# Kernel optimization log

Measured on AMD Instinct MI355X. Metric: run time of the kernel, lower is better.

The kernel has to match this reference:

```python
import jax, jax.numpy as jnp
import numpy as np

N = 20000      # num nodes
E = 320000     # num edges (avg degree 16)
F_IN = 518     # object_feature_dim
D = 128        # node_embedding_dim (= GAT out_channels)
ED = 32        # edge_embedding_dim
R = 26         # num_relations
H = 4          # GAT heads (concat=False -> mean over heads)
HID = 256      # node_encoder hidden


def _gat_layer(x, src, dst, ea, lin, lin_e, att_s, att_d, att_e, bias):
    """PyG GATConv: add_self_loops=True (fill_value='mean'), concat=False, negative_slope=0.2."""
    n = x.shape[0]
    ones = jnp.ones((src.shape[0],), x.dtype)
    cnt = jax.ops.segment_sum(ones, dst, num_segments=n)                    # [N]
    loop_ea = jax.ops.segment_sum(ea, dst, num_segments=n) / jnp.maximum(cnt, 1.0)[:, None]
    idx = jnp.arange(n)
    s = jnp.concatenate([src, idx])
    d = jnp.concatenate([dst, idx])
    ea2 = jnp.concatenate([ea, loop_ea], axis=0)                            # [E+N, ED]
    h = (x @ lin).reshape(n, H, D)                                          # [N,H,D]
    a_s = jnp.einsum('nhd,hd->nh', h, att_s)                                # [N,H]
    a_d = jnp.einsum('nhd,hd->nh', h, att_d)
    e = (ea2 @ lin_e).reshape(-1, H, D)                                     # [E+N,H,D]
    a_e = jnp.einsum('ehd,hd->eh', e, att_e)
    alpha = jax.nn.leaky_relu(a_s[s] + a_d[d] + a_e, 0.2)                   # [E+N,H]
    amax = jax.ops.segment_max(alpha, d, num_segments=n)
    alpha = jnp.exp(alpha - amax[d])
    denom = jax.ops.segment_sum(alpha, d, num_segments=n)
    alpha = alpha / (denom[d] + 1e-16)                                      # segment softmax
    msg = h[s] * alpha[:, :, None]                                          # [E+N,H,D]
    out = jax.ops.segment_sum(msg, d, num_segments=n)                       # [N,H,D]
    return out.mean(axis=1) + bias                                          # concat=False


def setup_inputs() -> dict:
    key = jax.random.key(0)
    ks = jax.random.split(key, 18)
    g = lambda k, shp, s=0.05: jax.random.normal(k, shp, jnp.float32) * s
    return {
        'x': g(ks[0], (N, F_IN), 1.0),
        'edge_index': jax.random.randint(ks[1], (2, E), 0, N),
        'edge_type': jax.random.randint(ks[2], (E,), 0, R),
        'w1': g(ks[3], (F_IN, HID)), 'b1': jnp.zeros((HID,), jnp.float32),
        'w2': g(ks[4], (HID, D)),    'b2': jnp.zeros((D,), jnp.float32),
        'rel_emb': g(ks[5], (R, ED), 1.0),
        'lin1': g(ks[6], (D, H * D)), 'line1': g(ks[7], (ED, H * D)),
        'atts1': g(ks[8], (H, D)), 'attd1': g(ks[9], (H, D)), 'atte1': g(ks[10], (H, D)),
        'bias1': jnp.zeros((D,), jnp.float32),
        'lin2': g(ks[11], (D, H * D)), 'line2': g(ks[12], (ED, H * D)),
        'atts2': g(ks[13], (H, D)), 'attd2': g(ks[14], (H, D)), 'atte2': g(ks[15], (H, D)),
        'bias2': jnp.zeros((D,), jnp.float32),
    }


def reference(x, edge_index, edge_type, w1, b1, w2, b2, rel_emb,
              lin1, line1, atts1, attd1, atte1, bias1,
              lin2, line2, atts2, attd2, atte2, bias2):
    src, dst = edge_index[0], edge_index[1]
    # node encoder (dropout inactive in eval)
    h = jax.nn.relu(x @ w1 + b1) @ w2 + b2                                  # [N,D]
    ea = rel_emb[edge_type]                                                 # [E,ED]
    h = jax.nn.relu(_gat_layer(h, src, dst, ea, lin1, line1, atts1, attd1, atte1, bias1))
    h = jax.nn.relu(_gat_layer(h, src, dst, ea, lin2, line2, atts2, attd2, atte2, bias2))
    return h
```

## Files before the change

kernel.cpp:

```cpp
#include <hip/hip_runtime.h>
#include <math.h>

#define N_NODES 20000
#define MP      20032
#define N_EDGES 320000
#define F_IN    518
#define HIDDEN  256
#define DIM     128
#define NH      4

typedef __attribute__((ext_vector_type(8))) short bf16x8;
typedef __attribute__((ext_vector_type(4))) float f32x4;
typedef unsigned short ushort_t;

__device__ __forceinline__ float lrelu02(float x) { return x > 0.f ? x : 0.2f * x; }

__device__ __forceinline__ void gl_lds16(const void* g, void* l) {
    __builtin_amdgcn_global_load_lds(
        (const __attribute__((address_space(1))) unsigned int*)g,
        (__attribute__((address_space(3))) unsigned int*)l, 16, 0, 0);
}

__device__ __forceinline__ unsigned int hi16(float v) { return __float_as_uint(v) >> 16; }
__device__ __forceinline__ unsigned int lo16(float v) {
    unsigned int h = __float_as_uint(v) & 0xFFFF0000u;
    return __float_as_uint(v - __uint_as_float(h)) >> 16;
}
__device__ __forceinline__ unsigned int rnd16(float v) {
    unsigned int u = __float_as_uint(v);
    return (u + 0x7FFFu + ((u >> 16) & 1u)) >> 16;
}
__device__ __forceinline__ float bfl(unsigned int u) { return __uint_as_float(u << 16); }
__device__ __forceinline__ float bfh(unsigned int u) { return __uint_as_float(u & 0xFFFF0000u); }

__global__ __launch_bounds__(256, 4) void gemm_mfma_v2(
    const ushort_t* __restrict__ Ah, const ushort_t* __restrict__ Al,
    const ushort_t* __restrict__ Bh, const ushort_t* __restrict__ Bl,
    const float* __restrict__ bias,
    int M, int K8, int N, int act,
    float* __restrict__ Cf,
    ushort_t* __restrict__ Ch, ushort_t* __restrict__ Cl,
    ushort_t* __restrict__ Cb,
    ushort_t* __restrict__ Ca)
{
    __shared__ __align__(16) ushort_t lds[12288];
    const int tid = threadIdx.x;
    const int w = tid >> 6, lane = tid & 63;
    const int row0 = blockIdx.y * 64, col0 = blockIdx.x * 128;
    const int nkb = K8 >> 2;
    const int m16 = lane & 15, q = lane >> 4;
    const bool use_al = (Al != nullptr);

    f32x4 acc[4][2] = {};

    for (int kb = 0; kb < nkb; ++kb) {
        const size_t kc = (size_t)(kb * 4 + w);
        const size_t aoff = (kc * MP + row0) * 8 + lane * 8;
        const size_t boff = (kc * N + col0) * 8 + lane * 8;
        gl_lds16(Ah + aoff, &lds[w * 512]);
        if (use_al) gl_lds16(Al + aoff, &lds[2048 + w * 512]);
        gl_lds16(Bh + boff,       &lds[4096 + w * 1024]);
        gl_lds16(Bh + boff + 512, &lds[4096 + w * 1024 + 512]);
        gl_lds16(Bl + boff,       &lds[8192 + w * 1024]);
        gl_lds16(Bl + boff + 512, &lds[8192 + w * 1024 + 512]);
        __syncthreads();

        bf16x8 fah[4], fal[4], fbh[2], fbl[2];
        const int fa = q * 512 + m16 * 8;
        #pragma unroll
        for (int mi = 0; mi < 4; ++mi) {
            fah[mi] = *(const bf16x8*)&lds[fa + mi * 128];
            if (use_al) fal[mi] = *(const bf16x8*)&lds[2048 + fa + mi * 128];
        }
        const int fb = q * 1024 + (w * 32 + m16) * 8;
        #pragma unroll
        for (int ni = 0; ni < 2; ++ni) {
            fbh[ni] = *(const bf16x8*)&lds[4096 + fb + ni * 128];
            fbl[ni] = *(const bf16x8*)&lds[8192 + fb + ni * 128];
        }
        #pragma unroll
        for (int mi = 0; mi < 4; ++mi)
            #pragma unroll
            for (int ni = 0; ni < 2; ++ni) {
                acc[mi][ni] = __builtin_amdgcn_mfma_f32_16x16x32_bf16(fah[mi], fbh[ni], acc[mi][ni], 0, 0, 0);
                acc[mi][ni] = __builtin_amdgcn_mfma_f32_16x16x32_bf16(fah[mi], fbl[ni], acc[mi][ni], 0, 0, 0);
            }
        if (use_al) {
            #pragma unroll
            for (int mi = 0; mi < 4; ++mi)
                #pragma unroll
                for (int ni = 0; ni < 2; ++ni)
                    acc[mi][ni] = __builtin_amdgcn_mfma_f32_16x16x32_bf16(fal[mi], fbh[ni], acc[mi][ni], 0, 0, 0);
        }
        __syncthreads();
    }

    #pragma unroll
    for (int ni = 0; ni < 2; ++ni) {
        const int col = col0 + w * 32 + ni * 16 + m16;
        const float bb = bias ? bias[col] : 0.f;
        #pragma unroll
        for (int mi = 0; mi < 4; ++mi) {
            #pragma unroll
            for (int r = 0; r < 4; ++r) {
                const int row = row0 + mi * 16 + q * 4 + r;
                if (row < M) {
                    float v = acc[mi][ni][r] + bb;
                    if (act) v = fmaxf(v, 0.f);
                    if (Cf) Cf[(size_t)row * N + col] = v;
                    if (Cb) Cb[(size_t)row * N + col] = (ushort_t)rnd16(v);
                    const size_t p = (((size_t)(col >> 3)) * MP + row) * 8 + (col & 7);
                    if (Ch) { Ch[p] = (ushort_t)hi16(v); Cl[p] = (ushort_t)lo16(v); }
                    if (Ca) Ca[p] = (ushort_t)rnd16(v);
                }
            }
        }
    }
}

__global__ __launch_bounds__(256, 3) void enc_fused_kernel(
    const ushort_t* __restrict__ Ah, const ushort_t* __restrict__ Al,
    const ushort_t* __restrict__ B1h, const ushort_t* __restrict__ B1l,
    const ushort_t* __restrict__ B2h, const ushort_t* __restrict__ B2l,
    const float* __restrict__ b1, const float* __restrict__ b2,
    float* __restrict__ Cf, ushort_t* __restrict__ Ca)
{
    __shared__ __align__(16) ushort_t lds[24576];
    const int tid = threadIdx.x;
    const int w = tid >> 6, lane = tid & 63;
    const int row0 = blockIdx.x * 64;
    const int m16 = lane & 15, q = lane >> 4;

    f32x4 acc1[4][4] = {};
    for (int kb = 0; kb < 17; ++kb) {
        const size_t kc = (size_t)(kb * 4 + w);
        const size_t aoff = (kc * MP + row0) * 8 + lane * 8;
        const size_t boff = kc * 2048 + lane * 8;
        gl_lds16(Ah + aoff, &lds[w * 512]);
        gl_lds16(Al + aoff, &lds[2048 + w * 512]);
        #pragma unroll
        for (int u = 0; u < 4; ++u) {
            gl_lds16(B1h + boff + u * 512, &lds[4096 + w * 2048 + u * 512]);
            gl_lds16(B1l + boff + u * 512, &lds[12288 + w * 2048 + u * 512]);
        }
        __syncthreads();

        bf16x8 fah[4], fal[4], fbh[4], fbl[4];
        const int fa = q * 512 + m16 * 8;
        #pragma unroll
        for (int mi = 0; mi < 4; ++mi) {
            fah[mi] = *(const bf16x8*)&lds[fa + mi * 128];
            fal[mi] = *(const bf16x8*)&lds[2048 + fa + mi * 128];
        }
        #pragma unroll
        for (int ni = 0; ni < 4; ++ni) {
            const int fb = q * 2048 + (ni * 64 + w * 16 + m16) * 8;
            fbh[ni] = *(const bf16x8*)&lds[4096 + fb];
            fbl[ni] = *(const bf16x8*)&lds[12288 + fb];
        }
        #pragma unroll
        for (int mi = 0; mi < 4; ++mi)
            #pragma unroll
            for (int ni = 0; ni < 4; ++ni) {
                acc1[mi][ni] = __builtin_amdgcn_mfma_f32_16x16x32_bf16(fah[mi], fbh[ni], acc1[mi][ni], 0, 0, 0);
                acc1[mi][ni] = __builtin_amdgcn_mfma_f32_16x16x32_bf16(fah[mi], fbl[ni], acc1[mi][ni], 0, 0, 0);
                acc1[mi][ni] = __builtin_amdgcn_mfma_f32_16x16x32_bf16(fal[mi], fbh[ni], acc1[mi][ni], 0, 0, 0);
            }
        __syncthreads();
    }

    float b1c[4];
    #pragma unroll
    for (int ni = 0; ni < 4; ++ni) b1c[ni] = b1[ni * 64 + w * 16 + m16];

    f32x4 acc2[4][2] = {};
    const int kc2l = w * 2 + (m16 >> 3);
    const int k7 = m16 & 7;
    for (int st = 0; st < 4; ++st) {
        #pragma unroll
        for (int mi = 0; mi < 4; ++mi)
            #pragma unroll
            for (int r = 0; r < 4; ++r) {
                const float v = fmaxf(acc1[mi][st][r] + b1c[st], 0.f);
                const int ad = kc2l * 512 + (mi * 16 + q * 4 + r) * 8 + k7;
                lds[ad] = (ushort_t)hi16(v);
                lds[4096 + ad] = (ushort_t)lo16(v);
            }
        #pragma unroll
        for (int c = 0; c < 2; ++c) {
            const size_t bo = (size_t)(st * 8 + w * 2 + c) * 1024 + lane * 8;
            const int dl = (w * 2 + c) * 1024;
            gl_lds16(B2h + bo,       &lds[8192 + dl]);
            gl_lds16(B2h + bo + 512, &lds[8192 + dl + 512]);
            gl_lds16(B2l + bo,       &lds[16384 + dl]);
            gl_lds16(B2l + bo + 512, &lds[16384 + dl + 512]);
        }
        __syncthreads();

        #pragma unroll
        for (int kb2 = 0; kb2 < 2; ++kb2) {
            bf16x8 ah[4], al[4], bh[2], bl[2];
            const int fa2 = (kb2 * 4 + q) * 512 + m16 * 8;
            #pragma unroll
            for (int mi = 0; mi < 4; ++mi) {
                ah[mi] = *(const bf16x8*)&lds[fa2 + mi * 128];
                al[mi] = *(const bf16x8*)&lds[4096 + fa2 + mi * 128];
            }
            #pragma unroll
            for (int ni = 0; ni < 2; ++ni) {
                const int fb2 = (kb2 * 4 + q) * 1024 + (w * 32 + ni * 16 + m16) * 8;
                bh[ni] = *(const bf16x8*)&lds[8192 + fb2];
                bl[ni] = *(const bf16x8*)&lds[16384 + fb2];
            }
            #pragma unroll
            for (int mi = 0; mi < 4; ++mi)
                #pragma unroll
                for (int ni = 0; ni < 2; ++ni) {
                    acc2[mi][ni] = __builtin_amdgcn_mfma_f32_16x16x32_bf16(ah[mi], bh[ni], acc2[mi][ni], 0, 0, 0);
                    acc2[mi][ni] = __builtin_amdgcn_mfma_f32_16x16x32_bf16(ah[mi], bl[ni], acc2[mi][ni], 0, 0, 0);
                    acc2[mi][ni] = __builtin_amdgcn_mfma_f32_16x16x32_bf16(al[mi], bh[ni], acc2[mi][ni], 0, 0, 0);
                }
        }
        __syncthreads();
    }

    #pragma unroll
    for (int ni = 0; ni < 2; ++ni) {
        const int col = w * 32 + ni * 16 + m16;
        const float bb = b2[col];
        #pragma unroll
        for (int mi = 0; mi < 4; ++mi) {
            #pragma unroll
            for (int r = 0; r < 4; ++r) {
                const int row = row0 + mi * 16 + q * 4 + r;
                if (row < N_NODES) {
                    const float v = acc2[mi][ni][r] + bb;
                    Cf[(size_t)row * DIM + col] = v;
                    const size_t p = (((size_t)(col >> 3)) * MP + row) * 8 + (col & 7);
                    Ca[p] = (ushort_t)rnd16(v);
                }
            }
        }
    }
}

__global__ __launch_bounds__(256) void conv_a_t_kernel(
    const float* __restrict__ x, ushort_t* __restrict__ xh, ushort_t* __restrict__ xl)
{
    __shared__ float tile[64][68];
    const int tid = threadIdx.x;
    const int r0 = blockIdx.x * 64;
    const int c0 = blockIdx.y * 64;

    #pragma unroll
    for (int it = 0; it < 4; ++it) {
        const int r = (tid >> 4) + it * 16;
        const int c = (tid & 15) * 4;
        const int gr = r0 + r, gc = c0 + c;
        float4 v = {0.f, 0.f, 0.f, 0.f};
        if (gr < N_NODES) {
            if (gc + 3 < F_IN) {
                v = *(const float4*)(x + (size_t)gr * F_IN + gc);
            } else {
                float tmp[4] = {0.f, 0.f, 0.f, 0.f};
                #pragma unroll
                for (int u = 0; u < 4; ++u)
                    if (gc + u < F_IN) tmp[u] = x[(size_t)gr * F_IN + gc + u];
                v.x = tmp[0]; v.y = tmp[1]; v.z = tmp[2]; v.w = tmp[3];
            }
        }
        tile[r][c] = v.x; tile[r][c+1] = v.y; tile[r][c+2] = v.z; tile[r][c+3] = v.w;
    }
    __syncthreads();

    const int k8l = tid >> 5;
    const int k8 = (c0 >> 3) + k8l;
    if (k8 >= 68) return;
    const int rr = (tid & 31) * 2;
    #pragma unroll
    for (int u = 0; u < 2; ++u) {
        const int r = rr + u;
        unsigned int hp[4], lp[4];
        #pragma unroll
        for (int i = 0; i < 4; ++i) {
            const float v0 = tile[r][k8l * 8 + 2 * i];
            const float v1 = tile[r][k8l * 8 + 2 * i + 1];
            hp[i] = (hi16(v1) << 16) | hi16(v0);
            lp[i] = (lo16(v1) << 16) | lo16(v0);
        }
        const size_t p = ((size_t)k8 * MP + r0 + r) * 8;
        *(uint4*)(xh + p) = make_uint4(hp[0], hp[1], hp[2], hp[3]);
        *(uint4*)(xl + p) = make_uint4(lp[0], lp[1], lp[2], lp[3]);
    }
}

#define W1_T (68 * 256 * 8)
#define W2_T (32 * 128 * 8)
#define L_T  (16 * 512 * 8)
__global__ __launch_bounds__(256) void conv_w_all_kernel(
    const float* __restrict__ w1, const float* __restrict__ w2,
    const float* __restrict__ l0, const float* __restrict__ l1,
    ushort_t* __restrict__ w1h, ushort_t* __restrict__ w1l,
    ushort_t* __restrict__ w2h, ushort_t* __restrict__ w2l,
    ushort_t* __restrict__ l0h, ushort_t* __restrict__ l0l,
    ushort_t* __restrict__ l1h, ushort_t* __restrict__ l1l)
{
    int idx = blockIdx.x * 256 + threadIdx.x;
    const float* w; ushort_t *bh, *bl; int K, N, local;
    if (idx < W1_T) { w = w1; bh = w1h; bl = w1l; K = F_IN; N = HIDDEN; local = idx; }
    else if (idx < W1_T + W2_T) { w = w2; bh = w2h; bl = w2l; K = HIDDEN; N = DIM; local = idx - W1_T; }
    else if (idx < W1_T + W2_T + L_T) { w = l0; bh = l0h; bl = l0l; K = DIM; N = 512; local = idx - W1_T - W2_T; }
    else if (idx < W1_T + W2_T + 2 * L_T) { w = l1; bh = l1h; bl = l1l; K = DIM; N = 512; local = idx - W1_T - W2_T - L_T; }
    else return;
    const int j = local & 7;
    const int rem = local >> 3;
    const int n = rem % N;
    const int k = (rem / N) * 8 + j;
    const float v = (k < K) ? w[(size_t)k * N + n] : 0.f;
    bh[local] = (ushort_t)hi16(v);
    bl[local] = (ushort_t)lo16(v);
}

__global__ __launch_bounds__(256) void wa2_kernel(
    const float* __restrict__ lin0, const float* __restrict__ lin1,
    const float* __restrict__ atts0, const float* __restrict__ attd0,
    const float* __restrict__ atts1, const float* __restrict__ attd1,
    float* __restrict__ wa_s0, float* __restrict__ wa_d0,
    float* __restrict__ wa_s1, float* __restrict__ wa_d1)
{
    const int wrk = blockIdx.x * 256 + threadIdx.x;
    if (wrk >= 2048) return;
    const int L = wrk >> 10;
    const int sd = (wrk >> 9) & 1;
    const int p = wrk & 511;
    const int h = p >> 7, d = p & 127;
    const float* lin = L ? lin1 : lin0;
    const float* av = L ? (sd ? attd1 : atts1) : (sd ? attd0 : atts0);
    float* out = L ? (sd ? wa_d1 : wa_s1) : (sd ? wa_d0 : wa_s0);
    const float* lp = lin + (size_t)d * (NH * DIM) + h * DIM;
    const float* ap = av + h * DIM;
    float acc = 0.f;
    #pragma unroll 8
    for (int i = 0; i < DIM; ++i) acc += lp[i] * ap[i];
    out[h * DIM + d] = acc;
}

__global__ __launch_bounds__(256) void as_ad_kernel(
    const float* __restrict__ xb, const float* __restrict__ wa_s,
    const float* __restrict__ wa_d, float* __restrict__ a_s, float* __restrict__ a_d)
{
    const int gw = blockIdx.x * 4 + (threadIdx.x >> 6);
    const int lane = threadIdx.x & 63;
    if (gw >= N_NODES * NH) return;
    const int n = gw >> 2, h = gw & 3;
    const float* hp = xb + (size_t)n * DIM;
    float2 hv = *(const float2*)(hp + lane * 2);
    float2 sv = *(const float2*)(wa_s + h * DIM + lane * 2);
    float2 dv = *(const float2*)(wa_d + h * DIM + lane * 2);
    float s = hv.x * sv.x + hv.y * sv.y;
    float d = hv.x * dv.x + hv.y * dv.y;
    #pragma unroll
    for (int off = 32; off > 0; off >>= 1) {
        s += __shfl_down(s, off);
        d += __shfl_down(d, off);
    }
    if (lane == 0) { a_s[n * 4 + h] = s; a_d[n * 4 + h] = d; }
}

__global__ __launch_bounds__(128) void rel_table2_kernel(
    const float* __restrict__ rel_emb,
    const float* __restrict__ line0, const float* __restrict__ atte0,
    const float* __restrict__ line1, const float* __restrict__ atte1,
    float* __restrict__ table)
{
    __shared__ float we[32][NH];
    const int L = blockIdx.x;
    const float* line = L ? line1 : line0;
    const float* atte = L ? atte1 : atte0;
    float* tab = table + L * 128;
    const int tid = threadIdx.x;
    const int k = tid >> 2, h = tid & 3;
    float acc = 0.f;
    for (int d = 0; d < DIM; ++d)
        acc += line[(size_t)k * (NH * DIM) + h * DIM + d] * atte[h * DIM + d];
    we[k][h] = acc;
    __syncthreads();
    if (tid < 26 * NH) {
        int r = tid >> 2, hh = tid & 3;
        float t = 0.f;
        for (int kk = 0; kk < 32; ++kk) t += rel_emb[r * 32 + kk] * we[kk][hh];
        tab[r * 4 + hh] = t;
    }
}

__global__ __launch_bounds__(256) void hist_kernel(
    const int* __restrict__ dst, int* __restrict__ cnt)
{
    const int e = blockIdx.x * blockDim.x + threadIdx.x;
    if (e >= N_EDGES) return;
    atomicAdd(&cnt[dst[e]], 1);
}

__global__ __launch_bounds__(1024) void scan_kernel(
    const int* __restrict__ cnt, int* __restrict__ ptr, int* __restrict__ ptr_copy)
{
    __shared__ int tsum[1024];
    const int tid = threadIdx.x;
    const int CH = 20;
    const int base = tid * CH;
    int s = 0;
    #pragma unroll
    for (int i = 0; i < CH; ++i) {
        int idx = base + i;
        if (idx < N_NODES) s += cnt[idx];
    }
    tsum[tid] = s;
    __syncthreads();
    for (int off = 1; off < 1024; off <<= 1) {
        int v = (tid >= off) ? tsum[tid - off] : 0;
        __syncthreads();
        tsum[tid] += v;
        __syncthreads();
    }
    int run = (tid == 0) ? 0 : tsum[tid - 1];
    #pragma unroll
    for (int i = 0; i < CH; ++i) {
        int idx = base + i;
        if (idx < N_NODES) {
            ptr[idx] = run;
            ptr_copy[idx] = run;
            run += cnt[idx];
        }
    }
    if (tid == 0) ptr[N_NODES] = N_EDGES;
}

__global__ __launch_bounds__(256) void scatter_kernel(
    const int* __restrict__ src, const int* __restrict__ dst, const int* __restrict__ etype,
    int* __restrict__ ptr_copy, int2* __restrict__ se, int* __restrict__ dcsr)
{
    const int e = blockIdx.x * blockDim.x + threadIdx.x;
    if (e >= N_EDGES) return;
    const int d = dst[e];
    const int pos = atomicAdd(&ptr_copy[d], 1);
    se[pos] = make_int2(src[e], etype[e]);
    dcsr[pos] = d;
}

__global__ __launch_bounds__(256) void edge_p_kernel(
    const int2* __restrict__ se, const int* __restrict__ dcsr,
    const float* __restrict__ a_s, const float* __restrict__ a_d,
    const float* __restrict__ table, float* __restrict__ p4)
{
    const int j0 = (blockIdx.x * 256 + threadIdx.x) * 2;
    const int2 eA = se[j0], eB = se[j0 + 1];
    const int dA = dcsr[j0], dB = dcsr[j0 + 1];
    const float4 asA = *(const float4*)(a_s + eA.x * 4);
    const float4 asB = *(const float4*)(a_s + eB.x * 4);
    const float4 adA = *(const float4*)(a_d + dA * 4);
    const float4 adB = *(const float4*)(a_d + dB * 4);
    const float4 tA  = *(const float4*)(table + eA.y * 4);
    const float4 tB  = *(const float4*)(table + eB.y * 4);
    float4 oA, oB;
    oA.x = __expf(lrelu02(asA.x + adA.x + tA.x));
    oA.y = __expf(lrelu02(asA.y + adA.y + tA.y));
    oA.z = __expf(lrelu02(asA.z + adA.z + tA.z));
    oA.w = __expf(lrelu02(asA.w + adA.w + tA.w));
    oB.x = __expf(lrelu02(asB.x + adB.x + tB.x));
    oB.y = __expf(lrelu02(asB.y + adB.y + tB.y));
    oB.z = __expf(lrelu02(asB.z + adB.z + tB.z));
    oB.w = __expf(lrelu02(asB.w + adB.w + tB.w));
    *(float4*)(p4 + (size_t)j0 * 4)     = oA;
    *(float4*)(p4 + (size_t)j0 * 4 + 4) = oB;
}

__device__ __forceinline__ void acc8(float acc[8], float p, const uint4 g)
{
    acc[0] += p * bfl(g.x); acc[1] += p * bfh(g.x);
    acc[2] += p * bfl(g.y); acc[3] += p * bfh(g.y);
    acc[4] += p * bfl(g.z); acc[5] += p * bfh(g.z);
    acc[6] += p * bfl(g.w); acc[7] += p * bfh(g.w);
}

__device__ __forceinline__ void agg_loop(
    int beg, int end, int n, int head, int cbase,
    const int2* __restrict__ se, const float* __restrict__ p4,
    const float* __restrict__ table, const float* __restrict__ a_s, float adh,
    const ushort_t* __restrict__ hb, float acc[8], float& dh)
{
    const uint4 gs = *(const uint4*)(hb + (size_t)n * 512 + cbase);

    float eh = 0.f;
    int j = beg;
    for (; j + 4 <= end; j += 4) {
        const int2 e0 = se[j],     e1 = se[j + 1];
        const int2 e2 = se[j + 2], e3 = se[j + 3];
        const float* pj = p4 + ((size_t)j * 4 + head);
        const float p0 = pj[0], p1 = pj[4], p2 = pj[8], p3 = pj[12];
        const uint4 g0 = *(const uint4*)(hb + (size_t)e0.x * 512 + cbase);
        const uint4 g1 = *(const uint4*)(hb + (size_t)e1.x * 512 + cbase);
        const uint4 g2 = *(const uint4*)(hb + (size_t)e2.x * 512 + cbase);
        const uint4 g3 = *(const uint4*)(hb + (size_t)e3.x * 512 + cbase);
        eh += (table[e0.y * 4 + head] + table[e1.y * 4 + head])
            + (table[e2.y * 4 + head] + table[e3.y * 4 + head]);
        dh += (p0 + p1) + (p2 + p3);
        acc8(acc, p0, g0); acc8(acc, p1, g1);
        acc8(acc, p2, g2); acc8(acc, p3, g3);
    }
    for (; j + 2 <= end; j += 2) {
        const int2 e0 = se[j], e1 = se[j + 1];
        const float* pj = p4 + ((size_t)j * 4 + head);
        const float p0 = pj[0], p1 = pj[4];
        const uint4 g0 = *(const uint4*)(hb + (size_t)e0.x * 512 + cbase);
        const uint4 g1 = *(const uint4*)(hb + (size_t)e1.x * 512 + cbase);
        eh += table[e0.y * 4 + head] + table[e1.y * 4 + head];
        dh += p0 + p1;
        acc8(acc, p0, g0); acc8(acc, p1, g1);
    }
    if (j < end) {
        const int2 e0 = se[j];
        const float p0 = p4[(size_t)j * 4 + head];
        const uint4 g0 = *(const uint4*)(hb + (size_t)e0.x * 512 + cbase);
        eh += table[e0.y * 4 + head];
        dh += p0;
        acc8(acc, p0, g0);
    }
    const float inv = 1.0f / fmaxf((float)(end - beg), 1.0f);
    const float ps = __expf(lrelu02(a_s[n * 4 + head] + adh + eh * inv));
    dh += ps;
    acc8(acc, ps, gs);
}

__global__ __launch_bounds__(256) void node_agg_f_kernel(
    const int* __restrict__ ptr, const int2* __restrict__ se,
    const float* __restrict__ p4, const float* __restrict__ table,
    const float* __restrict__ a_s, const float* __restrict__ a_d,
    const ushort_t* __restrict__ hb,
    const float* __restrict__ bias, ushort_t* __restrict__ oa,
    const float* __restrict__ wa_s2, const float* __restrict__ wa_d2,
    float* __restrict__ a_s2, float* __restrict__ a_d2)
{
    const int n = blockIdx.x * 4 + (threadIdx.x >> 6);
    const int lane = threadIdx.x & 63;
    if (n >= N_NODES) return;
    const int beg = ptr[n], end = ptr[n + 1];
    const int head = lane >> 4;
    const int cbase = lane * 8;
    const float adh = a_d[n * 4 + head];

    float acc[8] = {};
    float dh = 0.f;
    agg_loop(beg, end, n, head, cbase, se, p4, table, a_s, adh, hb, acc, dh);

    const float ih = 0.25f / (dh + 1e-16f);
    float t[8];
    #pragma unroll
    for (int k = 0; k < 8; ++k) {
        t[k] = acc[k] * ih;
        t[k] += __shfl_xor(t[k], 16);
        t[k] += __shfl_xor(t[k], 32);
    }
    if (lane < 16) {
        const float4 b0 = *(const float4*)(bias + cbase);
        const float4 b1 = *(const float4*)(bias + cbase + 4);
        float o[8];
        o[0] = fmaxf(t[0] + b0.x, 0.f); o[1] = fmaxf(t[1] + b0.y, 0.f);
        o[2] = fmaxf(t[2] + b0.z, 0.f); o[3] = fmaxf(t[3] + b0.w, 0.f);
        o[4] = fmaxf(t[4] + b1.x, 0.f); o[5] = fmaxf(t[5] + b1.y, 0.f);
        o[6] = fmaxf(t[6] + b1.z, 0.f); o[7] = fmaxf(t[7] + b1.w, 0.f);
        unsigned int up[4];
        #pragma unroll
        for (int i = 0; i < 4; ++i)
            up[i] = (rnd16(o[2*i+1]) << 16) | rnd16(o[2*i]);
        *(uint4*)(oa + ((size_t)lane * MP + n) * 8) = make_uint4(up[0], up[1], up[2], up[3]);
        float pss[4] = {0,0,0,0}, pdd[4] = {0,0,0,0};
        #pragma unroll
        for (int h = 0; h < NH; ++h) {
            const float* ws = wa_s2 + h * DIM + cbase;
            const float* wd = wa_d2 + h * DIM + cbase;
            #pragma unroll
            for (int i = 0; i < 8; ++i) {
                pss[h] += o[i] * ws[i];
                pdd[h] += o[i] * wd[i];
            }
        }
        #pragma unroll
        for (int m = 1; m < 16; m <<= 1) {
            #pragma unroll
            for (int h = 0; h < NH; ++h) {
                pss[h] += __shfl_xor(pss[h], m);
                pdd[h] += __shfl_xor(pdd[h], m);
            }
        }
        if (lane == 0) {
            float4 vs = {pss[0], pss[1], pss[2], pss[3]};
            float4 vd = {pdd[0], pdd[1], pdd[2], pdd[3]};
            *(float4*)(a_s2 + n * 4) = vs;
            *(float4*)(a_d2 + n * 4) = vd;
        }
    }
}

__global__ __launch_bounds__(256) void node_agg_s_kernel(
    const int* __restrict__ ptr, const int2* __restrict__ se,
    const float* __restrict__ p4, const float* __restrict__ table,
    const float* __restrict__ a_s, const float* __restrict__ a_d,
    const ushort_t* __restrict__ hb,
    const float* __restrict__ bias, float* __restrict__ outf)
{
    const int n = blockIdx.x * 4 + (threadIdx.x >> 6);
    const int lane = threadIdx.x & 63;
    if (n >= N_NODES) return;
    const int beg = ptr[n], end = ptr[n + 1];
    const int head = lane >> 4;
    const int cbase = lane * 8;
    const float adh = a_d[n * 4 + head];

    float acc[8] = {};
    float dh = 0.f;
    agg_loop(beg, end, n, head, cbase, se, p4, table, a_s, adh, hb, acc, dh);

    const float ih = 0.25f / (dh + 1e-16f);
    float t[8];
    #pragma unroll
    for (int k = 0; k < 8; ++k) {
        t[k] = acc[k] * ih;
        t[k] += __shfl_xor(t[k], 16);
        t[k] += __shfl_xor(t[k], 32);
    }
    if (lane < 16) {
        const float4 b0 = *(const float4*)(bias + cbase);
        const float4 b1 = *(const float4*)(bias + cbase + 4);
        float4 v0, v1;
        v0.x = fmaxf(t[0] + b0.x, 0.f); v0.y = fmaxf(t[1] + b0.y, 0.f);
        v0.z = fmaxf(t[2] + b0.z, 0.f); v0.w = fmaxf(t[3] + b0.w, 0.f);
        v1.x = fmaxf(t[4] + b1.x, 0.f); v1.y = fmaxf(t[5] + b1.y, 0.f);
        v1.z = fmaxf(t[6] + b1.z, 0.f); v1.w = fmaxf(t[7] + b1.w, 0.f);
        *(float4*)(outf + (size_t)n * DIM + cbase) = v0;
        *(float4*)(outf + (size_t)n * DIM + cbase + 4) = v1;
    }
}

extern "C" void kernel_launch(void* const* d_in, const int* in_sizes, int n_in,
                              void* d_out, int out_size, void* d_ws, size_t ws_size,
                              hipStream_t stream)
{
    const float* x       = (const float*)d_in[0];
    const int*   eidx    = (const int*)d_in[1];
    const int*   etype   = (const int*)d_in[2];
    const float* w1      = (const float*)d_in[3];
    const float* b1      = (const float*)d_in[4];
    const float* w2      = (const float*)d_in[5];
    const float* b2      = (const float*)d_in[6];
    const float* rel_emb = (const float*)d_in[7];
    const float* lin[2]  = {(const float*)d_in[8],  (const float*)d_in[14]};
    const float* line[2] = {(const float*)d_in[9],  (const float*)d_in[15]};
    const float* atts[2] = {(const float*)d_in[10], (const float*)d_in[16]};
    const float* attd[2] = {(const float*)d_in[11], (const float*)d_in[17]};
    const float* atte[2] = {(const float*)d_in[12], (const float*)d_in[18]};
    const float* bias[2] = {(const float*)d_in[13], (const float*)d_in[19]};
    const int* src = eidx;
    const int* dst = eidx + N_EDGES;

    char* base = (char*)d_ws;
    size_t off = 0;
    auto alloc = [&](size_t bytes) -> void* {
        void* p = base + off;
        off = (off + bytes + 255) & ~(size_t)255;
        return p;
    };
    ushort_t* xh  = (ushort_t*)alloc((size_t)68 * MP * 8 * 2);
    ushort_t* xl  = (ushort_t*)alloc((size_t)68 * MP * 8 * 2);
    ushort_t* x0a = (ushort_t*)alloc((size_t)16 * MP * 8 * 2);
    void* reg1    = alloc((size_t)16 * MP * 8 * 4);
    ushort_t* w1h = (ushort_t*)alloc(W1_T * 2);
    ushort_t* w1l = (ushort_t*)alloc(W1_T * 2);
    ushort_t* w2h = (ushort_t*)alloc(W2_T * 2);
    ushort_t* w2l = (ushort_t*)alloc(W2_T * 2);
    ushort_t* l0h = (ushort_t*)alloc(L_T * 2);
    ushort_t* l0l = (ushort_t*)alloc(L_T * 2);
    ushort_t* l1h = (ushort_t*)alloc(L_T * 2);
    ushort_t* l1l = (ushort_t*)alloc(L_T * 2);
    float* a_s0  = (float*)alloc(N_NODES * 4 * 4);
    float* a_d0  = (float*)alloc(N_NODES * 4 * 4);
    float* a_s1  = (float*)alloc(N_NODES * 4 * 4);
    float* a_d1  = (float*)alloc(N_NODES * 4 * 4);
    float* table = (float*)alloc(2 * 128 * 4);
    float* wa_s0 = (float*)alloc(512 * 4);
    float* wa_d0 = (float*)alloc(512 * 4);
    float* wa_s1 = (float*)alloc(512 * 4);
    float* wa_d1 = (float*)alloc(512 * 4);
    int*  cnt_i  = (int*)alloc(N_NODES * 4);
    int*  ptr    = (int*)alloc((N_NODES + 4) * 4);
    int*  ptrc   = (int*)alloc(N_NODES * 4);
    int2* se     = (int2*)alloc((size_t)N_EDGES * 8);
    int*  dcsr   = (int*)alloc((size_t)N_EDGES * 4);
    float* p4    = (float*)alloc((size_t)N_EDGES * 4 * 4);

    ushort_t* hb = xh;
    float* xbuf0 = (float*)reg1;
    ushort_t* x1a = (ushort_t*)reg1;

    const int mtiles = MP / 64;
    const int ep_grid = N_EDGES / 512;

    conv_a_t_kernel<<<dim3(MP / 64, 9), 256, 0, stream>>>(x, xh, xl);
    conv_w_all_kernel<<<(W1_T + W2_T + 2 * L_T + 255) / 256, 256, 0, stream>>>(
        w1, w2, lin[0], lin[1], w1h, w1l, w2h, w2l, l0h, l0l, l1h, l1l);
    wa2_kernel<<<8, 256, 0, stream>>>(lin[0], lin[1], atts[0], attd[0], atts[1], attd[1],
                                      wa_s0, wa_d0, wa_s1, wa_d1);
    rel_table2_kernel<<<2, 128, 0, stream>>>(rel_emb, line[0], atte[0], line[1], atte[1], table);

    hipMemsetAsync(cnt_i, 0, N_NODES * sizeof(int), stream);
    hist_kernel<<<(N_EDGES + 255) / 256, 256, 0, stream>>>(dst, cnt_i);
    scan_kernel<<<1, 1024, 0, stream>>>(cnt_i, ptr, ptrc);
    scatter_kernel<<<(N_EDGES + 255) / 256, 256, 0, stream>>>(src, dst, etype, ptrc, se, dcsr);

    enc_fused_kernel<<<mtiles, 256, 0, stream>>>(
        xh, xl, w1h, w1l, w2h, w2l, b1, b2, xbuf0, x0a);

    gemm_mfma_v2<<<dim3((NH * DIM) / 128, mtiles), 256, 0, stream>>>(
        x0a, nullptr, l0h, l0l, nullptr, N_NODES, 16, NH * DIM, 0, nullptr, nullptr, nullptr, hb, nullptr);
    as_ad_kernel<<<N_NODES, 256, 0, stream>>>(xbuf0, wa_s0, wa_d0, a_s0, a_d0);
    edge_p_kernel<<<ep_grid, 256, 0, stream>>>(se, dcsr, a_s0, a_d0, table, p4);
    node_agg_f_kernel<<<(N_NODES + 3) / 4, 256, 0, stream>>>(
        ptr, se, p4, table, a_s0, a_d0, hb, bias[0], x1a,
        wa_s1, wa_d1, a_s1, a_d1);

    gemm_mfma_v2<<<dim3((NH * DIM) / 128, mtiles), 256, 0, stream>>>(
        x1a, nullptr, l1h, l1l, nullptr, N_NODES, 16, NH * DIM, 0, nullptr, nullptr, nullptr, hb, nullptr);
    edge_p_kernel<<<ep_grid, 256, 0, stream>>>(se, dcsr, a_s1, a_d1, table + 128, p4);
    node_agg_s_kernel<<<(N_NODES + 3) / 4, 256, 0, stream>>>(
        ptr, se, p4, table + 128, a_s1, a_d1, hb, bias[1], (float*)d_out);
}
```

Measured before the change: 412.9 us.

## Fuse first GAT projection GEMM into encoder kernel and unroll aggregation by 8

The encoder kernel now stages its bf16 output tile in LDS and multiplies it directly by the layer-1 projection weights, writing the 512-wide bf16 features itself. This removes a separate GEMM launch and the round trip of the intermediate activation through global memory. Launch bounds drop to 2 blocks per CU to make room for the extra accumulators. The aggregation loop is also unrolled to 8 edges per step so more gathers are in flight at once, at the cost of more registers. The row-bounds check on stores is dropped, so correctness relies on the padded MP-row buffers.

```diff
diff --git a/kernel.cpp b/kernel.cpp
--- a/kernel.cpp
+++ b/kernel.cpp
@@ -118,12 +118,13 @@
     }
 }
 
-__global__ __launch_bounds__(256, 3) void enc_fused_kernel(
+__global__ __launch_bounds__(256, 2) void enc_fused_kernel(
     const ushort_t* __restrict__ Ah, const ushort_t* __restrict__ Al,
     const ushort_t* __restrict__ B1h, const ushort_t* __restrict__ B1l,
     const ushort_t* __restrict__ B2h, const ushort_t* __restrict__ B2l,
+    const ushort_t* __restrict__ B3h, const ushort_t* __restrict__ B3l,
     const float* __restrict__ b1, const float* __restrict__ b2,
-    float* __restrict__ Cf, ushort_t* __restrict__ Ca)
+    float* __restrict__ Cf, ushort_t* __restrict__ hbout)
 {
     __shared__ __align__(16) ushort_t lds[24576];
     const int tid = threadIdx.x;
@@ -226,18 +227,62 @@
 
     #pragma unroll
     for (int ni = 0; ni < 2; ++ni) {
-        const int col = w * 32 + ni * 16 + m16;
-        const float bb = b2[col];
+        const int colb = w * 32 + ni * 16 + m16;
+        const float bb = b2[colb];
+        const int kc3 = colb >> 3, k7b = colb & 7;
         #pragma unroll
         for (int mi = 0; mi < 4; ++mi) {
             #pragma unroll
             for (int r = 0; r < 4; ++r) {
-                const int row = row0 + mi * 16 + q * 4 + r;
-                if (row < N_NODES) {
-                    const float v = acc2[mi][ni][r] + bb;
-                    Cf[(size_t)row * DIM + col] = v;
-                    const size_t p = (((size_t)(col >> 3)) * MP + row) * 8 + (col & 7);
-                    Ca[p] = (ushort_t)rnd16(v);
+                const int rl = mi * 16 + q * 4 + r;
+                const float v = acc2[mi][ni][r] + bb;
+                Cf[(size_t)(row0 + rl) * DIM + colb] = v;
+                lds[kc3 * 512 + rl * 8 + k7b] = (ushort_t)rnd16(v);
+            }
+        }
+    }
+    __syncthreads();
+
+    for (int cp = 0; cp < 2; ++cp) {
+        f32x4 acc3[4][4] = {};
+        for (int kb3 = 0; kb3 < 4; ++kb3) {
+            const size_t bo = ((size_t)(kb3 * 4 + w) * 512 + cp * 256) * 8 + lane * 8;
+            #pragma unroll
+            for (int u = 0; u < 4; ++u) {
+                gl_lds16(B3h + bo + u * 512, &lds[8192 + w * 2048 + u * 512]);
+                gl_lds16(B3l + bo + u * 512, &lds[16384 + w * 2048 + u * 512]);
+            }
+            __syncthreads();
+
+            bf16x8 a3[4], b3h[4], b3l[4];
+            const int fa3 = (kb3 * 4 + q) * 512 + m16 * 8;
+            #pragma unroll
+            for (int mi = 0; mi < 4; ++mi)
+                a3[mi] = *(const bf16x8*)&lds[fa3 + mi * 128];
+            #pragma unroll
+            for (int ni = 0; ni < 4; ++ni) {
+                const int fb3 = q * 2048 + (w * 64 + ni * 16 + m16) * 8;
+                b3h[ni] = *(const bf16x8*)&lds[8192 + fb3];
+                b3l[ni] = *(const bf16x8*)&lds[16384 + fb3];
+            }
+            #pragma unroll
+            for (int mi = 0; mi < 4; ++mi)
+                #pragma unroll
+                for (int ni = 0; ni < 4; ++ni) {
+                    acc3[mi][ni] = __builtin_amdgcn_mfma_f32_16x16x32_bf16(a3[mi], b3h[ni], acc3[mi][ni], 0, 0, 0);
+                    acc3[mi][ni] = __builtin_amdgcn_mfma_f32_16x16x32_bf16(a3[mi], b3l[ni], acc3[mi][ni], 0, 0, 0);
+                }
+            __syncthreads();
+        }
+        #pragma unroll
+        for (int ni = 0; ni < 4; ++ni) {
+            const int col = cp * 256 + w * 64 + ni * 16 + m16;
+            #pragma unroll
+            for (int mi = 0; mi < 4; ++mi) {
+                #pragma unroll
+                for (int r = 0; r < 4; ++r) {
+                    const int row = row0 + mi * 16 + q * 4 + r;
+                    hbout[(size_t)row * 512 + col] = (ushort_t)rnd16(acc3[mi][ni][r]);
                 }
             }
         }
@@ -492,20 +537,24 @@
 
     float eh = 0.f;
     int j = beg;
-    for (; j + 4 <= end; j += 4) {
-        const int2 e0 = se[j],     e1 = se[j + 1];
-        const int2 e2 = se[j + 2], e3 = se[j + 3];
+    for (; j + 8 <= end; j += 8) {
+        int2 E[8];
+        #pragma unroll
+        for (int u = 0; u < 8; ++u) E[u] = se[j + u];
         const float* pj = p4 + ((size_t)j * 4 + head);
-        const float p0 = pj[0], p1 = pj[4], p2 = pj[8], p3 = pj[12];
-        const uint4 g0 = *(const uint4*)(hb + (size_t)e0.x * 512 + cbase);
-        const uint4 g1 = *(const uint4*)(hb + (size_t)e1.x * 512 + cbase);
-        const uint4 g2 = *(const uint4*)(hb + (size_t)e2.x * 512 + cbase);
-        const uint4 g3 = *(const uint4*)(hb + (size_t)e3.x * 512 + cbase);
-        eh += (table[e0.y * 4 + head] + table[e1.y * 4 + head])
-            + (table[e2.y * 4 + head] + table[e3.y * 4 + head]);
-        dh += (p0 + p1) + (p2 + p3);
-        acc8(acc, p0, g0); acc8(acc, p1, g1);
-        acc8(acc, p2, g2); acc8(acc, p3, g3);
+        float p[8];
+        #pragma unroll
+        for (int u = 0; u < 8; ++u) p[u] = pj[u * 4];
+        uint4 g[8];
+        #pragma unroll
+        for (int u = 0; u < 8; ++u)
+            g[u] = *(const uint4*)(hb + (size_t)E[u].x * 512 + cbase);
+        float ehs = 0.f, dhs = 0.f;
+        #pragma unroll
+        for (int u = 0; u < 8; ++u) { ehs += table[E[u].y * 4 + head]; dhs += p[u]; }
+        eh += ehs; dh += dhs;
+        #pragma unroll
+        for (int u = 0; u < 8; ++u) acc8(acc, p[u], g[u]);
     }
     for (; j + 2 <= end; j += 2) {
         const int2 e0 = se[j], e1 = se[j + 1];
@@ -671,7 +720,7 @@
     };
     ushort_t* xh  = (ushort_t*)alloc((size_t)68 * MP * 8 * 2);
     ushort_t* xl  = (ushort_t*)alloc((size_t)68 * MP * 8 * 2);
-    ushort_t* x0a = (ushort_t*)alloc((size_t)16 * MP * 8 * 2);
+    ushort_t* hb0 = (ushort_t*)alloc((size_t)MP * 512 * 2);
     void* reg1    = alloc((size_t)16 * MP * 8 * 4);
     ushort_t* w1h = (ushort_t*)alloc(W1_T * 2);
     ushort_t* w1l = (ushort_t*)alloc(W1_T * 2);
@@ -697,7 +746,6 @@
     int*  dcsr   = (int*)alloc((size_t)N_EDGES * 4);
     float* p4    = (float*)alloc((size_t)N_EDGES * 4 * 4);
 
-    ushort_t* hb = xh;
     float* xbuf0 = (float*)reg1;
     ushort_t* x1a = (ushort_t*)reg1;
 
@@ -717,19 +765,17 @@
     scatter_kernel<<<(N_EDGES + 255) / 256, 256, 0, stream>>>(src, dst, etype, ptrc, se, dcsr);
 
     enc_fused_kernel<<<mtiles, 256, 0, stream>>>(
-        xh, xl, w1h, w1l, w2h, w2l, b1, b2, xbuf0, x0a);
-
-    gemm_mfma_v2<<<dim3((NH * DIM) / 128, mtiles), 256, 0, stream>>>(
-        x0a, nullptr, l0h, l0l, nullptr, N_NODES, 16, NH * DIM, 0, nullptr, nullptr, nullptr, hb, nullptr);
+        xh, xl, w1h, w1l, w2h, w2l, l0h, l0l, b1, b2, xbuf0, hb0);
+
     as_ad_kernel<<<N_NODES, 256, 0, stream>>>(xbuf0, wa_s0, wa_d0, a_s0, a_d0);
     edge_p_kernel<<<ep_grid, 256, 0, stream>>>(se, dcsr, a_s0, a_d0, table, p4);
     node_agg_f_kernel<<<(N_NODES + 3) / 4, 256, 0, stream>>>(
-        ptr, se, p4, table, a_s0, a_d0, hb, bias[0], x1a,
+        ptr, se, p4, table, a_s0, a_d0, hb0, bias[0], x1a,
         wa_s1, wa_d1, a_s1, a_d1);
 
     gemm_mfma_v2<<<dim3((NH * DIM) / 128, mtiles), 256, 0, stream>>>(
-        x1a, nullptr, l1h, l1l, nullptr, N_NODES, 16, NH * DIM, 0, nullptr, nullptr, nullptr, hb, nullptr);
+        x1a, nullptr, l1h, l1l, nullptr, N_NODES, 16, NH * DIM, 0, nullptr, nullptr, nullptr, hb0, nullptr);
     edge_p_kernel<<<ep_grid, 256, 0, stream>>>(se, dcsr, a_s1, a_d1, table + 128, p4);
     node_agg_s_kernel<<<(N_NODES + 3) / 4, 256, 0, stream>>>(
-        ptr, se, p4, table + 128, a_s1, a_d1, hb, bias[1], (float*)d_out);
-}
+        ptr, se, p4, table + 128, a_s1, a_d1, hb0, bias[1], (float*)d_out);
+}
```

New measurement: 403.4 us. 1.02x faster.
